# Optimization experiments

Measured on AMD Instinct MI355X. Metric: run time of the kernel, lower is better.

Reference implementation:

```python
import jax, jax.numpy as jnp
import numpy as np

HIDDEN = 2048
INTER = 1408
NUM_EXPERTS = 8
TOP_K = 2


def setup_inputs() -> dict:
    key = jax.random.key(0)
    k_x, k_rw, k_gu, k_dn = jax.random.split(key, 4)
    x = jax.random.normal(k_x, (2, 2048, HIDDEN), dtype=jnp.float32)
    router_weight = jax.random.normal(k_rw, (NUM_EXPERTS, HIDDEN), dtype=jnp.float32)
    gate_up_proj = jax.random.normal(k_gu, (NUM_EXPERTS, 2 * INTER, HIDDEN), dtype=jnp.float32) * 0.02
    down_proj = jax.random.normal(k_dn, (NUM_EXPERTS, HIDDEN, INTER), dtype=jnp.float32) * 0.02
    return {"x": x, "router_weight": router_weight, "gate_up_proj": gate_up_proj, "down_proj": down_proj}


def reference(x, router_weight, gate_up_proj, down_proj):
    E = router_weight.shape[0]
    xf = x.reshape(-1, x.shape[-1])  # [T, D]
    # Router: logits -> float32 softmax -> top-k -> renormalize
    logits = jnp.einsum('td,ed->te', xf, router_weight)
    scores = jax.nn.softmax(logits.astype(jnp.float32), axis=-1)
    topv, topi = jax.lax.top_k(scores, TOP_K)          # [T, K]
    topv = topv / jnp.sum(topv, axis=-1, keepdims=True)
    topv = topv.astype(logits.dtype)
    # Combine weights per (token, expert): zero for unselected experts,
    # so dense per-expert compute below reproduces the sparse dispatch math.
    comb = jnp.einsum('tk,tke->te', topv, jax.nn.one_hot(topi, E, dtype=topv.dtype))  # [T, E]
    # Per-expert SwiGLU FFN, dense over experts
    gu = jnp.einsum('td,efd->etf', xf, gate_up_proj)    # [E, T, 2*inter]
    gate, up = jnp.split(gu, 2, axis=-1)
    h = jax.nn.silu(gate) * up                          # [E, T, inter]
    eo = jnp.einsum('eti,edi->etd', h, down_proj)       # [E, T, D]
    out = jnp.einsum('etd,te->td', eo, comb)            # [T, D]
    return out
```

## Files before the change

### kernel.cpp

```cpp
#include <hip/hip_runtime.h>
#include <hip/hip_bf16.h>
#include <stdint.h>

#define HIDDEN 2048
#define INTER  1408
#define NE     8
#define NTOK   4096
#define MAXTILES 72

typedef __attribute__((ext_vector_type(8))) short short8;
typedef __attribute__((ext_vector_type(4))) float f32x4;

typedef const __attribute__((address_space(1))) unsigned char* gp1_t;
typedef __attribute__((address_space(3))) unsigned char* lp3_t;

__device__ __forceinline__ void lds_cp16(const void* g, void* l) {
    __builtin_amdgcn_global_load_lds((gp1_t)g, (lp3_t)l, 16, 0, 0);
}

__device__ __forceinline__ short8 ldswz(const __hip_bfloat16 (*S)[64], int r, int col) {
    return *(const short8*)&S[r][(((col >> 3) ^ (r & 7)) << 3)];
}

__device__ __forceinline__ float bf2f(short s) {
    union { float f; unsigned u; } u; u.u = ((unsigned)(unsigned short)s) << 16; return u.f;
}

#define C0 (NTOK * HIDDEN / 4)
#define C1 (NE * 2 * INTER * HIDDEN / 4)
#define C2 (NE * HIDDEN * INTER / 4)
__global__ void cvt_all_kernel(const float* __restrict__ x, const float* __restrict__ gu,
                               const float* __restrict__ dn,
                               __hip_bfloat16* __restrict__ xb, __hip_bfloat16* __restrict__ gub,
                               __hip_bfloat16* __restrict__ dnb) {
    long c = (long)blockIdx.x * blockDim.x + threadIdx.x;
    const float* s; __hip_bfloat16* d; long o;
    if (c < C0)           { s = x;  d = xb;  o = c; }
    else if (c < C0 + C1) { s = gu; d = gub; o = c - C0; }
    else                  { s = dn; d = dnb; o = c - C0 - C1; }
    o *= 4;
    float4 v = *(const float4*)(s + o);
    *(__hip_bfloat162*)(d + o)     = __float22bfloat162_rn(make_float2(v.x, v.y));
    *(__hip_bfloat162*)(d + o + 2) = __float22bfloat162_rn(make_float2(v.z, v.w));
}

__global__ void router_kernel(const float* __restrict__ x, const float* __restrict__ rw,
                              int* __restrict__ counts, int* __restrict__ topk_e,
                              float* __restrict__ topk_w) {
    int wave = threadIdx.x >> 6;
    int lane = threadIdx.x & 63;
    int t = blockIdx.x * 4 + wave;
    const float* xr = x + (size_t)t * HIDDEN;
    float acc[NE] = {0.f,0.f,0.f,0.f,0.f,0.f,0.f,0.f};
    for (int i = lane; i < HIDDEN; i += 64) {
        float xi = xr[i];
        #pragma unroll
        for (int e = 0; e < NE; ++e) acc[e] += xi * rw[e * HIDDEN + i];
    }
    #pragma unroll
    for (int e = 0; e < NE; ++e) {
        #pragma unroll
        for (int off = 32; off > 0; off >>= 1) acc[e] += __shfl_xor(acc[e], off, 64);
    }
    if (lane == 0) {
        int i1 = 0; float v1 = acc[0];
        for (int e = 1; e < NE; ++e) if (acc[e] > v1) { v1 = acc[e]; i1 = e; }
        int i2 = -1; float v2 = -3.0e38f;
        for (int e = 0; e < NE; ++e) if (e != i1 && acc[e] > v2) { v2 = acc[e]; i2 = e; }
        float w1 = 1.f / (1.f + expf(v2 - v1));
        float w2 = 1.f - w1;
        topk_e[t * 2 + 0] = i1; topk_e[t * 2 + 1] = i2;
        topk_w[t * 2 + 0] = w1; topk_w[t * 2 + 1] = w2;
        atomicAdd(&counts[i1], 1);
        atomicAdd(&counts[i2], 1);
    }
}

__global__ void scan_kernel(const int* __restrict__ counts, int* __restrict__ offsets,
                            int* __restrict__ cursor, int* __restrict__ tiles,
                            int* __restrict__ n_tiles) {
    if (threadIdx.x == 0) {
        int s = 0, nt = 0;
        for (int e = 0; e < NE; ++e) {
            offsets[e] = s; cursor[e] = s;
            int c = counts[e]; s += c;
            for (int mt = 0; mt * 128 < c; ++mt) tiles[nt++] = (e << 16) | mt;
        }
        n_tiles[0] = nt;
    }
}

__global__ void scatter_kernel(const int* __restrict__ topk_e, const float* __restrict__ topk_w,
                               int* __restrict__ cursor, int* __restrict__ slot_tid,
                               float* __restrict__ slot_w, int* __restrict__ tok2slot) {
    int k = blockIdx.x * blockDim.x + threadIdx.x;
    if (k >= NTOK * 2) return;
    int e = topk_e[k];
    int slot = atomicAdd(&cursor[e], 1);
    slot_tid[slot] = k >> 1;
    slot_w[slot]   = topk_w[k];
    tok2slot[k]    = slot;
}

__global__ __launch_bounds__(256) void gemm1_kernel(
    const __hip_bfloat16* __restrict__ xb,
    const __hip_bfloat16* __restrict__ gub,
    const int* __restrict__ counts, const int* __restrict__ offsets,
    const int* __restrict__ tiles, const int* __restrict__ n_tiles,
    const int* __restrict__ slot_tid, const float* __restrict__ slot_w,
    __hip_bfloat16* __restrict__ h)
{
    const int ti = blockIdx.y;
    if (ti >= n_tiles[0]) return;
    const int tile = tiles[ti];
    const int e  = tile >> 16;
    const int mt = tile & 0xffff;
    const int nt = blockIdx.x;
    const int count = counts[e];
    const int off = offsets[e];

    __shared__ __hip_bfloat16 As[128][64];
    __shared__ __hip_bfloat16 Bs[128][64];

    const int tid  = threadIdx.x;
    const int wave = tid >> 6;
    const int lane = tid & 63;
    const int wm = wave >> 1, wn = wave & 1;

    const __hip_bfloat16* asrc[4];
    const __hip_bfloat16* bsrc[4];
    #pragma unroll
    for (int j = 0; j < 4; ++j) {
        int fs  = j * 256 + tid;
        int row = fs >> 3;
        int c8  = (fs & 7) ^ (row & 7);
        int rg  = mt * 128 + row;
        int rc  = rg < count ? rg : count - 1;
        int tok = slot_tid[off + rc];
        asrc[j] = xb + (size_t)tok * HIDDEN + c8 * 8;
        int within = row & 63, sel = within >> 5, idx = within & 31;
        int hc  = nt * 64 + (row >> 6) * 32 + idx;
        int grow = sel ? (INTER + hc) : hc;
        bsrc[j] = gub + ((size_t)e * 2 * INTER + grow) * HIDDEN + c8 * 8;
    }

    f32x4 acc[4][4];
    #pragma unroll
    for (int mi = 0; mi < 4; ++mi)
        #pragma unroll
        for (int ni = 0; ni < 4; ++ni) acc[mi][ni] = (f32x4)0.f;

    const int fr = lane & 15;
    const int fk = (lane >> 4) * 8;

    for (int k0 = 0; k0 < HIDDEN; k0 += 64) {
        #pragma unroll
        for (int j = 0; j < 4; ++j) {
            lds_cp16(asrc[j] + k0, (__hip_bfloat16*)As + (j * 256 + tid) * 8);
            lds_cp16(bsrc[j] + k0, (__hip_bfloat16*)Bs + (j * 256 + tid) * 8);
        }
        __syncthreads();
        #pragma unroll
        for (int kk = 0; kk < 64; kk += 32) {
            short8 a[4], b[4];
            #pragma unroll
            for (int mi = 0; mi < 4; ++mi) a[mi] = ldswz(As, wm * 64 + mi * 16 + fr, kk + fk);
            #pragma unroll
            for (int ni = 0; ni < 4; ++ni) b[ni] = ldswz(Bs, wn * 64 + ni * 16 + fr, kk + fk);
            #pragma unroll
            for (int mi = 0; mi < 4; ++mi)
                #pragma unroll
                for (int ni = 0; ni < 4; ++ni)
                    acc[mi][ni] = __builtin_amdgcn_mfma_f32_16x16x32_bf16(a[mi], b[ni], acc[mi][ni], 0, 0, 0);
        }
        __syncthreads();
    }

    #pragma unroll
    for (int mi = 0; mi < 4; ++mi) {
        #pragma unroll
        for (int r = 0; r < 4; ++r) {
            int row = wm * 64 + mi * 16 + (lane >> 4) * 4 + r;
            int rg  = mt * 128 + row;
            if (rg < count) {
                float wgt = slot_w[off + rg];
                size_t base = (size_t)(off + rg) * INTER + nt * 64 + wn * 32;
                #pragma unroll
                for (int ni = 0; ni < 2; ++ni) {
                    float g = acc[mi][ni][r];
                    float u = acc[mi][ni + 2][r];
                    float hv = g / (1.f + __expf(-g)) * u * wgt;
                    h[base + ni * 16 + fr] = __float2bfloat16(hv);
                }
            }
        }
    }
}

__global__ __launch_bounds__(256) void gemm2_kernel(
    const __hip_bfloat16* __restrict__ h,
    const __hip_bfloat16* __restrict__ dnb,
    const int* __restrict__ counts, const int* __restrict__ offsets,
    const int* __restrict__ tiles, const int* __restrict__ n_tiles,
    __hip_bfloat16* __restrict__ eo)
{
    const int ti = blockIdx.y;
    if (ti >= n_tiles[0]) return;
    const int tile = tiles[ti];
    const int e  = tile >> 16;
    const int mt = tile & 0xffff;
    const int nt = blockIdx.x;
    const int count = counts[e];
    const int off = offsets[e];

    __shared__ __hip_bfloat16 As[128][64];
    __shared__ __hip_bfloat16 Bs[128][64];

    const int tid  = threadIdx.x;
    const int wave = tid >> 6;
    const int lane = tid & 63;
    const int wm = wave >> 1, wn = wave & 1;

    const __hip_bfloat16* asrc[4];
    const __hip_bfloat16* bsrc[4];
    #pragma unroll
    for (int j = 0; j < 4; ++j) {
        int fs  = j * 256 + tid;
        int row = fs >> 3;
        int c8  = (fs & 7) ^ (row & 7);
        asrc[j] = h + (size_t)(off + mt * 128 + row) * INTER + c8 * 8;
        bsrc[j] = dnb + ((size_t)e * HIDDEN + nt * 128 + row) * INTER + c8 * 8;
    }

    f32x4 acc[4][4];
    #pragma unroll
    for (int mi = 0; mi < 4; ++mi)
        #pragma unroll
        for (int ni = 0; ni < 4; ++ni) acc[mi][ni] = (f32x4)0.f;

    const int fr = lane & 15;
    const int fk = (lane >> 4) * 8;

    for (int k0 = 0; k0 < INTER; k0 += 64) {
        #pragma unroll
        for (int j = 0; j < 4; ++j) {
            lds_cp16(asrc[j] + k0, (__hip_bfloat16*)As + (j * 256 + tid) * 8);
            lds_cp16(bsrc[j] + k0, (__hip_bfloat16*)Bs + (j * 256 + tid) * 8);
        }
        __syncthreads();
        #pragma unroll
        for (int kk = 0; kk < 64; kk += 32) {
            short8 a[4], b[4];
            #pragma unroll
            for (int mi = 0; mi < 4; ++mi) a[mi] = ldswz(As, wm * 64 + mi * 16 + fr, kk + fk);
            #pragma unroll
            for (int ni = 0; ni < 4; ++ni) b[ni] = ldswz(Bs, wn * 64 + ni * 16 + fr, kk + fk);
            #pragma unroll
            for (int mi = 0; mi < 4; ++mi)
                #pragma unroll
                for (int ni = 0; ni < 4; ++ni)
                    acc[mi][ni] = __builtin_amdgcn_mfma_f32_16x16x32_bf16(a[mi], b[ni], acc[mi][ni], 0, 0, 0);
        }
        __syncthreads();
    }

    #pragma unroll
    for (int mi = 0; mi < 4; ++mi) {
        #pragma unroll
        for (int r = 0; r < 4; ++r) {
            int row = wm * 64 + mi * 16 + (lane >> 4) * 4 + r;
            int rg  = mt * 128 + row;
            if (rg < count) {
                size_t base = (size_t)(off + rg) * HIDDEN + nt * 128 + wn * 64;
                #pragma unroll
                for (int ni = 0; ni < 4; ++ni)
                    eo[base + ni * 16 + fr] = __float2bfloat16(acc[mi][ni][r]);
            }
        }
    }
}

__global__ void combine_kernel(const __hip_bfloat16* __restrict__ eo,
                               const int* __restrict__ tok2slot,
                               float* __restrict__ out) {
    int idx = blockIdx.x * blockDim.x + threadIdx.x;
    int t = idx >> 8;
    int c = (idx & 255) * 8;
    int s1 = tok2slot[t * 2], s2 = tok2slot[t * 2 + 1];
    short8 v1 = *(const short8*)(eo + (size_t)s1 * HIDDEN + c);
    short8 v2 = *(const short8*)(eo + (size_t)s2 * HIDDEN + c);
    float4 o0, o1;
    o0.x = bf2f(v1[0]) + bf2f(v2[0]); o0.y = bf2f(v1[1]) + bf2f(v2[1]);
    o0.z = bf2f(v1[2]) + bf2f(v2[2]); o0.w = bf2f(v1[3]) + bf2f(v2[3]);
    o1.x = bf2f(v1[4]) + bf2f(v2[4]); o1.y = bf2f(v1[5]) + bf2f(v2[5]);
    o1.z = bf2f(v1[6]) + bf2f(v2[6]); o1.w = bf2f(v1[7]) + bf2f(v2[7]);
    float* op = out + (size_t)t * HIDDEN + c;
    *(float4*)op = o0;
    *(float4*)(op + 4) = o1;
}

extern "C" void kernel_launch(void* const* d_in, const int* in_sizes, int n_in,
                              void* d_out, int out_size, void* d_ws, size_t ws_size,
                              hipStream_t stream)
{
    (void)in_sizes; (void)n_in; (void)ws_size; (void)out_size;
    const float* x  = (const float*)d_in[0];
    const float* rw = (const float*)d_in[1];
    const float* gu = (const float*)d_in[2];
    const float* dn = (const float*)d_in[3];

    char* p = (char*)d_ws;
    auto take = [&](size_t bytes) { char* r = p; p += (bytes + 255) & ~(size_t)255; return r; };
    __hip_bfloat16* xb  = (__hip_bfloat16*)take((size_t)NTOK * HIDDEN * 2);
    __hip_bfloat16* gub = (__hip_bfloat16*)take((size_t)NE * 2 * INTER * HIDDEN * 2);
    __hip_bfloat16* dnb = (__hip_bfloat16*)take((size_t)NE * HIDDEN * INTER * 2);
    __hip_bfloat16* hbuf= (__hip_bfloat16*)take((size_t)(2 * NTOK + 128) * INTER * 2);
    int*   counts   = (int*)take(64);
    int*   offsets  = (int*)take(64);
    int*   cursor   = (int*)take(64);
    int*   ntile    = (int*)take(64);
    int*   tiles    = (int*)take(MAXTILES * 4);
    int*   topk_e   = (int*)take((size_t)NTOK * 2 * 4);
    float* topk_w   = (float*)take((size_t)NTOK * 2 * 4);
    int*   slot_tid = (int*)take((size_t)(2 * NTOK + 128) * 4);
    float* slot_w   = (float*)take((size_t)(2 * NTOK + 128) * 4);
    int*   tok2slot = (int*)take((size_t)NTOK * 2 * 4);
    __hip_bfloat16* eo = gub;

    hipMemsetAsync(counts, 0, 64, stream);

    cvt_all_kernel<<<dim3((C0 + C1 + C2) / 256), 256, 0, stream>>>(x, gu, dn, xb, gub, dnb);

    router_kernel<<<dim3(NTOK / 4), 256, 0, stream>>>(x, rw, counts, topk_e, topk_w);
    scan_kernel<<<dim3(1), 64, 0, stream>>>(counts, offsets, cursor, tiles, ntile);
    scatter_kernel<<<dim3((NTOK * 2) / 256), 256, 0, stream>>>(topk_e, topk_w, cursor,
                                                               slot_tid, slot_w, tok2slot);

    gemm1_kernel<<<dim3(INTER / 64, MAXTILES), 256, 0, stream>>>(
        xb, gub, counts, offsets, tiles, ntile, slot_tid, slot_w, hbuf);
    gemm2_kernel<<<dim3(HIDDEN / 128, MAXTILES), 256, 0, stream>>>(
        hbuf, dnb, counts, offsets, tiles, ntile, eo);
    combine_kernel<<<dim3(NTOK * HIDDEN / 8 / 256), 256, 0, stream>>>(
        eo, tok2slot, (float*)d_out);
}
```

Measured before the change: 730.3 us.

## Switch expert GEMMs to 32x32x16 MFMA and fuse x conversion into router

Both grouped GEMM kernels now use 32x32x16 bf16 MFMA tiles instead of 16x16x32. Each wave issues fewer LDS fragment loads per MFMA and holds accumulators in 16-wide vectors, with the gate/up and epilogue index mapping rewritten to match. Separately, the fp32-to-bf16 conversion of x moves into the router kernel, which already reads x, and the router now loads x and the router weights as float4. This saves one full read of x and a branch in the weight conversion kernel, at the cost of new epilogue layouts that must match the 32x32 MFMA output format.

```diff
diff --git a/kernel.cpp b/kernel.cpp
--- a/kernel.cpp
+++ b/kernel.cpp
@@ -9,7 +9,7 @@
 #define MAXTILES 72
 
 typedef __attribute__((ext_vector_type(8))) short short8;
-typedef __attribute__((ext_vector_type(4))) float f32x4;
+typedef __attribute__((ext_vector_type(16))) float f32x16;
 
 typedef const __attribute__((address_space(1))) unsigned char* gp1_t;
 typedef __attribute__((address_space(3))) unsigned char* lp3_t;
@@ -26,18 +26,14 @@
     union { float f; unsigned u; } u; u.u = ((unsigned)(unsigned short)s) << 16; return u.f;
 }
 
-#define C0 (NTOK * HIDDEN / 4)
 #define C1 (NE * 2 * INTER * HIDDEN / 4)
 #define C2 (NE * HIDDEN * INTER / 4)
-__global__ void cvt_all_kernel(const float* __restrict__ x, const float* __restrict__ gu,
-                               const float* __restrict__ dn,
-                               __hip_bfloat16* __restrict__ xb, __hip_bfloat16* __restrict__ gub,
-                               __hip_bfloat16* __restrict__ dnb) {
+__global__ void cvt_w_kernel(const float* __restrict__ gu, const float* __restrict__ dn,
+                             __hip_bfloat16* __restrict__ gub, __hip_bfloat16* __restrict__ dnb) {
     long c = (long)blockIdx.x * blockDim.x + threadIdx.x;
     const float* s; __hip_bfloat16* d; long o;
-    if (c < C0)           { s = x;  d = xb;  o = c; }
-    else if (c < C0 + C1) { s = gu; d = gub; o = c - C0; }
-    else                  { s = dn; d = dnb; o = c - C0 - C1; }
+    if (c < C1) { s = gu; d = gub; o = c; }
+    else        { s = dn; d = dnb; o = c - C1; }
     o *= 4;
     float4 v = *(const float4*)(s + o);
     *(__hip_bfloat162*)(d + o)     = __float22bfloat162_rn(make_float2(v.x, v.y));
@@ -46,16 +42,23 @@
 
 __global__ void router_kernel(const float* __restrict__ x, const float* __restrict__ rw,
                               int* __restrict__ counts, int* __restrict__ topk_e,
-                              float* __restrict__ topk_w) {
+                              float* __restrict__ topk_w, __hip_bfloat16* __restrict__ xb) {
     int wave = threadIdx.x >> 6;
     int lane = threadIdx.x & 63;
     int t = blockIdx.x * 4 + wave;
-    const float* xr = x + (size_t)t * HIDDEN;
+    const float4* xr = (const float4*)(x + (size_t)t * HIDDEN);
+    __hip_bfloat16* xbr = xb + (size_t)t * HIDDEN;
     float acc[NE] = {0.f,0.f,0.f,0.f,0.f,0.f,0.f,0.f};
-    for (int i = lane; i < HIDDEN; i += 64) {
-        float xi = xr[i];
-        #pragma unroll
-        for (int e = 0; e < NE; ++e) acc[e] += xi * rw[e * HIDDEN + i];
+    #pragma unroll
+    for (int c = lane; c < HIDDEN / 4; c += 64) {
+        float4 v = xr[c];
+        *(__hip_bfloat162*)(xbr + c * 4)     = __float22bfloat162_rn(make_float2(v.x, v.y));
+        *(__hip_bfloat162*)(xbr + c * 4 + 2) = __float22bfloat162_rn(make_float2(v.z, v.w));
+        #pragma unroll
+        for (int e = 0; e < NE; ++e) {
+            float4 w = ((const float4*)(rw + e * HIDDEN))[c];
+            acc[e] += v.x * w.x + v.y * w.y + v.z * w.z + v.w * w.w;
+        }
     }
     #pragma unroll
     for (int e = 0; e < NE; ++e) {
@@ -126,6 +129,8 @@
     const int wave = tid >> 6;
     const int lane = tid & 63;
     const int wm = wave >> 1, wn = wave & 1;
+    const int l31 = lane & 31;
+    const int fk  = (lane >> 5) * 8;
 
     const __hip_bfloat16* asrc[4];
     const __hip_bfloat16* bsrc[4];
@@ -144,14 +149,9 @@
         bsrc[j] = gub + ((size_t)e * 2 * INTER + grow) * HIDDEN + c8 * 8;
     }
 
-    f32x4 acc[4][4];
-    #pragma unroll
-    for (int mi = 0; mi < 4; ++mi)
-        #pragma unroll
-        for (int ni = 0; ni < 4; ++ni) acc[mi][ni] = (f32x4)0.f;
-
-    const int fr = lane & 15;
-    const int fk = (lane >> 4) * 8;
+    f32x16 accg[2], accu[2];
+    #pragma unroll
+    for (int mi = 0; mi < 2; ++mi) { accg[mi] = (f32x16)0.f; accu[mi] = (f32x16)0.f; }
 
     for (int k0 = 0; k0 < HIDDEN; k0 += 64) {
         #pragma unroll
@@ -161,37 +161,31 @@
         }
         __syncthreads();
         #pragma unroll
-        for (int kk = 0; kk < 64; kk += 32) {
-            short8 a[4], b[4];
-            #pragma unroll
-            for (int mi = 0; mi < 4; ++mi) a[mi] = ldswz(As, wm * 64 + mi * 16 + fr, kk + fk);
-            #pragma unroll
-            for (int ni = 0; ni < 4; ++ni) b[ni] = ldswz(Bs, wn * 64 + ni * 16 + fr, kk + fk);
-            #pragma unroll
-            for (int mi = 0; mi < 4; ++mi)
-                #pragma unroll
-                for (int ni = 0; ni < 4; ++ni)
-                    acc[mi][ni] = __builtin_amdgcn_mfma_f32_16x16x32_bf16(a[mi], b[ni], acc[mi][ni], 0, 0, 0);
+        for (int kk = 0; kk < 64; kk += 16) {
+            short8 a0 = ldswz(As, wm * 64 +      l31, kk + fk);
+            short8 a1 = ldswz(As, wm * 64 + 32 + l31, kk + fk);
+            short8 bg = ldswz(Bs, wn * 64 +      l31, kk + fk);
+            short8 bu = ldswz(Bs, wn * 64 + 32 + l31, kk + fk);
+            accg[0] = __builtin_amdgcn_mfma_f32_32x32x16_bf16(a0, bg, accg[0], 0, 0, 0);
+            accg[1] = __builtin_amdgcn_mfma_f32_32x32x16_bf16(a1, bg, accg[1], 0, 0, 0);
+            accu[0] = __builtin_amdgcn_mfma_f32_32x32x16_bf16(a0, bu, accu[0], 0, 0, 0);
+            accu[1] = __builtin_amdgcn_mfma_f32_32x32x16_bf16(a1, bu, accu[1], 0, 0, 0);
         }
         __syncthreads();
     }
 
     #pragma unroll
-    for (int mi = 0; mi < 4; ++mi) {
-        #pragma unroll
-        for (int r = 0; r < 4; ++r) {
-            int row = wm * 64 + mi * 16 + (lane >> 4) * 4 + r;
+    for (int mi = 0; mi < 2; ++mi) {
+        #pragma unroll
+        for (int reg = 0; reg < 16; ++reg) {
+            int row = wm * 64 + mi * 32 + (reg & 3) + 8 * (reg >> 2) + 4 * (lane >> 5);
             int rg  = mt * 128 + row;
             if (rg < count) {
                 float wgt = slot_w[off + rg];
-                size_t base = (size_t)(off + rg) * INTER + nt * 64 + wn * 32;
-                #pragma unroll
-                for (int ni = 0; ni < 2; ++ni) {
-                    float g = acc[mi][ni][r];
-                    float u = acc[mi][ni + 2][r];
-                    float hv = g / (1.f + __expf(-g)) * u * wgt;
-                    h[base + ni * 16 + fr] = __float2bfloat16(hv);
-                }
+                float g = accg[mi][reg];
+                float u = accu[mi][reg];
+                float hv = g / (1.f + __expf(-g)) * u * wgt;
+                h[(size_t)(off + rg) * INTER + nt * 64 + wn * 32 + l31] = __float2bfloat16(hv);
             }
         }
     }
@@ -220,6 +214,8 @@
     const int wave = tid >> 6;
     const int lane = tid & 63;
     const int wm = wave >> 1, wn = wave & 1;
+    const int l31 = lane & 31;
+    const int fk  = (lane >> 5) * 8;
 
     const __hip_bfloat16* asrc[4];
     const __hip_bfloat16* bsrc[4];
@@ -232,14 +228,11 @@
         bsrc[j] = dnb + ((size_t)e * HIDDEN + nt * 128 + row) * INTER + c8 * 8;
     }
 
-    f32x4 acc[4][4];
-    #pragma unroll
-    for (int mi = 0; mi < 4; ++mi)
-        #pragma unroll
-        for (int ni = 0; ni < 4; ++ni) acc[mi][ni] = (f32x4)0.f;
-
-    const int fr = lane & 15;
-    const int fk = (lane >> 4) * 8;
+    f32x16 acc[2][2];
+    #pragma unroll
+    for (int mi = 0; mi < 2; ++mi)
+        #pragma unroll
+        for (int nj = 0; nj < 2; ++nj) acc[mi][nj] = (f32x16)0.f;
 
     for (int k0 = 0; k0 < INTER; k0 += 64) {
         #pragma unroll
@@ -249,32 +242,29 @@
         }
         __syncthreads();
         #pragma unroll
-        for (int kk = 0; kk < 64; kk += 32) {
-            short8 a[4], b[4];
-            #pragma unroll
-            for (int mi = 0; mi < 4; ++mi) a[mi] = ldswz(As, wm * 64 + mi * 16 + fr, kk + fk);
-            #pragma unroll
-            for (int ni = 0; ni < 4; ++ni) b[ni] = ldswz(Bs, wn * 64 + ni * 16 + fr, kk + fk);
-            #pragma unroll
-            for (int mi = 0; mi < 4; ++mi)
-                #pragma unroll
-                for (int ni = 0; ni < 4; ++ni)
-                    acc[mi][ni] = __builtin_amdgcn_mfma_f32_16x16x32_bf16(a[mi], b[ni], acc[mi][ni], 0, 0, 0);
+        for (int kk = 0; kk < 64; kk += 16) {
+            short8 a0 = ldswz(As, wm * 64 +      l31, kk + fk);
+            short8 a1 = ldswz(As, wm * 64 + 32 + l31, kk + fk);
+            short8 b0 = ldswz(Bs, wn * 64 +      l31, kk + fk);
+            short8 b1 = ldswz(Bs, wn * 64 + 32 + l31, kk + fk);
+            acc[0][0] = __builtin_amdgcn_mfma_f32_32x32x16_bf16(a0, b0, acc[0][0], 0, 0, 0);
+            acc[0][1] = __builtin_amdgcn_mfma_f32_32x32x16_bf16(a0, b1, acc[0][1], 0, 0, 0);
+            acc[1][0] = __builtin_amdgcn_mfma_f32_32x32x16_bf16(a1, b0, acc[1][0], 0, 0, 0);
+            acc[1][1] = __builtin_amdgcn_mfma_f32_32x32x16_bf16(a1, b1, acc[1][1], 0, 0, 0);
         }
         __syncthreads();
     }
 
     #pragma unroll
-    for (int mi = 0; mi < 4; ++mi) {
-        #pragma unroll
-        for (int r = 0; r < 4; ++r) {
-            int row = wm * 64 + mi * 16 + (lane >> 4) * 4 + r;
+    for (int mi = 0; mi < 2; ++mi) {
+        #pragma unroll
+        for (int reg = 0; reg < 16; ++reg) {
+            int row = wm * 64 + mi * 32 + (reg & 3) + 8 * (reg >> 2) + 4 * (lane >> 5);
             int rg  = mt * 128 + row;
             if (rg < count) {
                 size_t base = (size_t)(off + rg) * HIDDEN + nt * 128 + wn * 64;
-                #pragma unroll
-                for (int ni = 0; ni < 4; ++ni)
-                    eo[base + ni * 16 + fr] = __float2bfloat16(acc[mi][ni][r]);
+                eo[base +      l31] = __float2bfloat16(acc[mi][0][reg]);
+                eo[base + 32 + l31] = __float2bfloat16(acc[mi][1][reg]);
             }
         }
     }
@@ -329,9 +319,9 @@
 
     hipMemsetAsync(counts, 0, 64, stream);
 
-    cvt_all_kernel<<<dim3((C0 + C1 + C2) / 256), 256, 0, stream>>>(x, gu, dn, xb, gub, dnb);
-
-    router_kernel<<<dim3(NTOK / 4), 256, 0, stream>>>(x, rw, counts, topk_e, topk_w);
+    cvt_w_kernel<<<dim3((C1 + C2) / 256), 256, 0, stream>>>(gu, dn, gub, dnb);
+
+    router_kernel<<<dim3(NTOK / 4), 256, 0, stream>>>(x, rw, counts, topk_e, topk_w, xb);
     scan_kernel<<<dim3(1), 64, 0, stream>>>(counts, offsets, cursor, tiles, ntile);
     scatter_kernel<<<dim3((NTOK * 2) / 256), 256, 0, stream>>>(topk_e, topk_w, cursor,
                                                                slot_tid, slot_w, tok2slot);
```

Result: faster. 691.1 us (-5.4%).
